# Kernel optimization log

Measured on AMD Instinct MI355X. Metric: run time of the kernel, lower is better.

Reference implementation:

```python
import jax, jax.numpy as jnp
import numpy as np


def setup_inputs() -> dict:
    key = jax.random.key(0)
    k1, k2, k3 = jax.random.split(key, 3)
    B, N, D, S = 256, 200000, 128, 256
    return {
        "query": jax.random.normal(k1, (B, D), dtype=jnp.float32),
        "keys": jax.random.normal(k2, (N, D), dtype=jnp.float32),
        "slots": jax.random.normal(k3, (N, S), dtype=jnp.float32),
        "k": 8,
    }


def reference(query, keys, slots, k):
    # FAISS IndexFlatIP exact search: inner-product scores over all stored keys.
    scores = jnp.einsum("bd,nd->bn", query, keys)          # [B, N]
    top_scores, top_idx = jax.lax.top_k(scores, k)          # [B, k]
    # Fused id->slot gather (replaces per-(query,neighbor) equality scans).
    retrieved_slots = slots[top_idx]                        # [B, k, slot_dim]
    return retrieved_slots, top_scores
```

## Files before the change

### kernel.cpp

```cpp
#include <hip/hip_runtime.h>

#define NQ    256
#define DD    128
#define NK    200000
#define SD    256
#define KTOP  8
#define CAP   1024

#define NCH   500
#define CHK   400
#define KST   80
#define NST   (CHK/KST)
#define KT    (KST/16)
static_assert(NCH * CHK == NK, "chunking must cover keys");

#define WS_A    0
#define WS_TAUF 65536
#define WS_TAU  66560
#define WS_CNT  67584
#define WS_FLAG 68608
#define WS_CAND 69632

#define NEG_INF (-3.402823466e+38f)

typedef __attribute__((ext_vector_type(8))) short short8;
typedef __attribute__((ext_vector_type(4))) float f32x4;

__device__ __forceinline__ unsigned f2bf(float f) {
    unsigned u = __float_as_uint(f);
    u += 0x7fffu + ((u >> 16) & 1u);
    return u >> 16;
}

__device__ __forceinline__ float dot128(const float4* __restrict__ qr,
                                        const float4* __restrict__ kr) {
    float s0 = 0.f, s1 = 0.f;
#pragma unroll
    for (int d = 0; d < 16; ++d) {
        float4 a = qr[d], b = kr[d];
        s0 = fmaf(a.x, b.x, s0); s0 = fmaf(a.y, b.y, s0);
        s0 = fmaf(a.z, b.z, s0); s0 = fmaf(a.w, b.w, s0);
    }
#pragma unroll
    for (int d = 16; d < 32; ++d) {
        float4 a = qr[d], b = kr[d];
        s1 = fmaf(a.x, b.x, s1); s1 = fmaf(a.y, b.y, s1);
        s1 = fmaf(a.z, b.z, s1); s1 = fmaf(a.w, b.w, s1);
    }
    return s0 + s1;
}

template <int T>
__device__ __forceinline__ void topk_insert(float (&vs)[T], int (&vi)[T],
                                            float &vmin, float s, int idx) {
    if (s <= vmin) return;
    bool done = false;
#pragma unroll
    for (int j = 0; j < T; ++j)
        if (!done && vs[j] == vmin) { vs[j] = s; vi[j] = idx; done = true; }
    float m = vs[0];
#pragma unroll
    for (int j = 1; j < T; ++j) m = fminf(m, vs[j]);
    vmin = m;
}

__device__ void finalize_write(int q, int t, float (&vs)[KTOP], int (&vi)[KTOP],
                               float vmin, float* ds, int* di,
                               const float* __restrict__ slots,
                               float* __restrict__ out) {
#pragma unroll
    for (int j = 0; j < KTOP; ++j) { ds[t * KTOP + j] = vs[j]; di[t * KTOP + j] = vi[j]; }
    __syncthreads();
    for (int step = 128; step >= 1; step >>= 1) {
        if (t < step) {
            for (int j = 0; j < KTOP; ++j)
                topk_insert<KTOP>(vs, vi, vmin, ds[(t + step) * KTOP + j],
                                  di[(t + step) * KTOP + j]);
#pragma unroll
            for (int j = 0; j < KTOP; ++j) { ds[t * KTOP + j] = vs[j]; di[t * KTOP + j] = vi[j]; }
        }
        __syncthreads();
    }
    if (t == 0) {
#pragma unroll
        for (int i = 0; i < KTOP; ++i)
#pragma unroll
            for (int j = 0; j < KTOP - 1 - i; ++j) {
                bool swp = (vs[j + 1] > vs[j]) ||
                           (vs[j + 1] == vs[j] && vi[j + 1] < vi[j]);
                if (swp) {
                    float tf = vs[j]; vs[j] = vs[j + 1]; vs[j + 1] = tf;
                    int   ti = vi[j]; vi[j] = vi[j + 1]; vi[j + 1] = ti;
                }
            }
#pragma unroll
        for (int j = 0; j < KTOP; ++j) { ds[j] = vs[j]; di[j] = vi[j]; }
    }
    __syncthreads();
    const float4* slots4 = (const float4*)slots;
    float4* out4 = (float4*)out;
    for (int f = t; f < KTOP * (SD / 4); f += 256) {
        int j = f >> 6, s4 = f & 63;
        out4[(size_t)q * (KTOP * SD / 4) + f] = slots4[(size_t)di[j] * (SD / 4) + s4];
    }
    if (t < KTOP)
        out[(size_t)NQ * KTOP * SD + q * KTOP + t] = ds[t];
}

__global__ __launch_bounds__(256) void prep(const float* __restrict__ query,
                                            char* __restrict__ ws) {
    __shared__ float qs[16 * DD];
    __shared__ float nrm[16][17];
    const int b = blockIdx.x, t = threadIdx.x;

    const float4* src = (const float4*)(query + (size_t)b * 16 * DD);
    float4* dst = (float4*)qs;
    for (int i = t; i < 512; i += 256) dst[i] = src[i];
    __syncthreads();

    {
        int r = t >> 4, p = t & 15;
        float s = 0.f;
#pragma unroll
        for (int j = 0; j < 8; ++j) { float v = qs[r * DD + p * 8 + j]; s = fmaf(v, v, s); }
        nrm[r][p] = s;
    }
    __syncthreads();
    if (t < 16) {
        float s = 0.f;
#pragma unroll
        for (int p = 0; p < 16; ++p) s += nrm[t][p];
        float tau = 3.2f * sqrtf(s);
        ((float*)(ws + WS_TAU))[b * 16 + t]  = tau;
        ((float*)(ws + WS_TAUF))[b * 16 + t] = tau - 1.0f;
    }
    if (b == 0) { ((int*)(ws + WS_CNT))[t] = 0; ((int*)(ws + WS_FLAG))[t] = 0; }

    {
        int c = t >> 6, l = t & 63, col = l & 15, quad = l >> 4;
        const float* row = qs + col * DD + c * 32 + quad * 8;
        int4 pk;
        pk.x = f2bf(row[0]) | (f2bf(row[1]) << 16);
        pk.y = f2bf(row[2]) | (f2bf(row[3]) << 16);
        pk.z = f2bf(row[4]) | (f2bf(row[5]) << 16);
        pk.w = f2bf(row[6]) | (f2bf(row[7]) << 16);
        ((int4*)(ws + WS_A))[(b * 4 + c) * 64 + l] = pk;
    }
}

__global__ __launch_bounds__(256, 2)
void phaseA(const float* __restrict__ keys, char* __restrict__ ws) {
    __shared__ __align__(16) char sm[KST * 256];

    const int tid = threadIdx.x;
    const int w = tid >> 6, lane = tid & 63;
    const int col = lane & 15, quad = lane >> 4;
    const int key0 = blockIdx.x * CHK;

    const short8* wsA = (const short8*)(ws + WS_A);
    short8 A[4][4];
#pragma unroll
    for (int at = 0; at < 4; ++at)
#pragma unroll
        for (int c = 0; c < 4; ++c)
            A[at][c] = wsA[((w * 4 + at) * 4 + c) * 64 + lane];

    const float* tauf = (const float*)(ws + WS_TAUF);
    float tf[4][4];
#pragma unroll
    for (int at = 0; at < 4; ++at)
#pragma unroll
        for (int r = 0; r < 4; ++r)
            tf[at][r] = tauf[w * 64 + at * 16 + quad * 4 + r];

    int* cnt  = (int*)(ws + WS_CNT);
    int* cand = (int*)(ws + WS_CAND);

    float4 rg[5][2];
#pragma unroll
    for (int i = 0; i < 5; ++i) {
        int u = tid + 256 * i, tc = u >> 6, l = u & 63;
        const float* p = keys + (size_t)(key0 + (tc >> 2) * 16 + (l & 15)) * DD
                              + (tc & 3) * 32 + (l >> 4) * 8;
        rg[i][0] = ((const float4*)p)[0];
        rg[i][1] = ((const float4*)p)[1];
    }

    for (int s = 0; s < NST; ++s) {
#pragma unroll
        for (int i = 0; i < 5; ++i) {
            int u = tid + 256 * i;
            int4 pk;
            pk.x = f2bf(rg[i][0].x) | (f2bf(rg[i][0].y) << 16);
            pk.y = f2bf(rg[i][0].z) | (f2bf(rg[i][0].w) << 16);
            pk.z = f2bf(rg[i][1].x) | (f2bf(rg[i][1].y) << 16);
            pk.w = f2bf(rg[i][1].z) | (f2bf(rg[i][1].w) << 16);
            *(int4*)(sm + (size_t)u * 16) = pk;
        }
        __syncthreads();
        if (s + 1 < NST) {
#pragma unroll
            for (int i = 0; i < 5; ++i) {
                int u = tid + 256 * i, tc = u >> 6, l = u & 63;
                const float* p = keys + (size_t)(key0 + (s + 1) * KST + (tc >> 2) * 16 + (l & 15)) * DD
                                      + (tc & 3) * 32 + (l >> 4) * 8;
                rg[i][0] = ((const float4*)p)[0];
                rg[i][1] = ((const float4*)p)[1];
            }
        }
        const short8* B = (const short8*)sm;
#pragma unroll
        for (int kt = 0; kt < KT; ++kt) {
            short8 b0 = B[(kt * 4 + 0) * 64 + lane];
            short8 b1 = B[(kt * 4 + 1) * 64 + lane];
            short8 b2 = B[(kt * 4 + 2) * 64 + lane];
            short8 b3 = B[(kt * 4 + 3) * 64 + lane];
            const int kidx = key0 + s * KST + kt * 16 + col;
#pragma unroll
            for (int at = 0; at < 4; ++at) {
                f32x4 acc = {0.f, 0.f, 0.f, 0.f};
                acc = __builtin_amdgcn_mfma_f32_16x16x32_bf16(A[at][0], b0, acc, 0, 0, 0);
                acc = __builtin_amdgcn_mfma_f32_16x16x32_bf16(A[at][1], b1, acc, 0, 0, 0);
                acc = __builtin_amdgcn_mfma_f32_16x16x32_bf16(A[at][2], b2, acc, 0, 0, 0);
                acc = __builtin_amdgcn_mfma_f32_16x16x32_bf16(A[at][3], b3, acc, 0, 0, 0);
#pragma unroll
                for (int r = 0; r < 4; ++r) {
                    if (acc[r] > tf[at][r]) {
                        int q = w * 64 + at * 16 + quad * 4 + r;
                        int p = atomicAdd(&cnt[q], 1);
                        if (p < CAP) cand[q * CAP + p] = kidx;
                    }
                }
            }
        }
        __syncthreads();
    }
}

__global__ __launch_bounds__(256)
void phaseB(const float* __restrict__ query, const float* __restrict__ keys,
            const float* __restrict__ slots, float* __restrict__ out,
            char* __restrict__ ws) {
    const int q = blockIdx.x, t = threadIdx.x;

    __shared__ float cs[CAP];
    __shared__ int   ci[CAP];
    __shared__ int   nAbove;
    __shared__ float ds[256 * KTOP];
    __shared__ int   di[256 * KTOP];

    if (t == 0) nAbove = 0;
    __syncthreads();

    const int m0 = ((const int*)(ws + WS_CNT))[q];
    const int m  = min(m0, CAP);
    const float tq = ((const float*)(ws + WS_TAU))[q];
    const int* cand = (const int*)(ws + WS_CAND) + (size_t)q * CAP;
    const float4* qr = (const float4*)(query + (size_t)q * DD);

    int myAbove = 0;
    for (int c = t; c < m; c += 256) {
        int id = cand[c];
        float s = dot128(qr, (const float4*)(keys + (size_t)id * DD));
        cs[c] = s; ci[c] = id;
        if (s >= tq) ++myAbove;
    }
    if (myAbove) atomicAdd(&nAbove, myAbove);
    __syncthreads();

    if (m0 > CAP || nAbove < KTOP) {
        if (t == 0) ((int*)(ws + WS_FLAG))[q] = 1;
        return;
    }

    float vs[KTOP]; int vi[KTOP]; float vmin = NEG_INF;
#pragma unroll
    for (int j = 0; j < KTOP; ++j) { vs[j] = NEG_INF; vi[j] = -1; }
    for (int c = t; c < m; c += 256)
        topk_insert<KTOP>(vs, vi, vmin, cs[c], ci[c]);

    finalize_write(q, t, vs, vi, vmin, ds, di, slots, out);
}

__global__ __launch_bounds__(256)
void fallback(const float* __restrict__ query, const float* __restrict__ keys,
              const float* __restrict__ slots, float* __restrict__ out,
              const char* __restrict__ ws) {
    const int q = blockIdx.x;
    if (((const int*)(ws + WS_FLAG))[q] == 0) return;
    const int t = threadIdx.x;

    __shared__ float ds[256 * KTOP];
    __shared__ int   di[256 * KTOP];

    float vs[KTOP]; int vi[KTOP]; float vmin = NEG_INF;
#pragma unroll
    for (int j = 0; j < KTOP; ++j) { vs[j] = NEG_INF; vi[j] = -1; }

    const float4* qr = (const float4*)(query + (size_t)q * DD);
    for (int id = t; id < NK; id += 256) {
        float s = dot128(qr, (const float4*)(keys + (size_t)id * DD));
        topk_insert<KTOP>(vs, vi, vmin, s, id);
    }
    finalize_write(q, t, vs, vi, vmin, ds, di, slots, out);
}

extern "C" void kernel_launch(void* const* d_in, const int* in_sizes, int n_in,
                              void* d_out, int out_size, void* d_ws, size_t ws_size,
                              hipStream_t stream) {
    const float* query = (const float*)d_in[0];
    const float* keys  = (const float*)d_in[1];
    const float* slots = (const float*)d_in[2];
    (void)in_sizes; (void)n_in; (void)out_size; (void)ws_size;
    char* ws = (char*)d_ws;

    hipLaunchKernelGGL(prep,     dim3(16),  dim3(256), 0, stream, query, ws);
    hipLaunchKernelGGL(phaseA,   dim3(NCH), dim3(256), 0, stream, keys, ws);
    hipLaunchKernelGGL(phaseB,   dim3(NQ),  dim3(256), 0, stream, query, keys, slots,
                       (float*)d_out, ws);
    hipLaunchKernelGGL(fallback, dim3(NQ),  dim3(256), 0, stream, query, keys, slots,
                       (float*)d_out, ws);
}
```

Measured before the change: 367.3 us.

## Double-buffer phaseA LDS stages and fold fallback into phaseB

phaseA now keeps two LDS buffers. The next stage is converted and written into the alternate buffer after the MFMA work, so each stage needs one barrier instead of two. The fallback kernel is removed and its brute-force scan is inlined into phaseB, which drops one kernel launch and the flag workspace. The cost is double the LDS per block, which could limit occupancy at 2 blocks per CU, and phaseB may now carry more register pressure.

```diff
diff --git a/kernel.cpp b/kernel.cpp
--- a/kernel.cpp
+++ b/kernel.cpp
@@ -12,13 +12,13 @@
 #define KST   80
 #define NST   (CHK/KST)
 #define KT    (KST/16)
+#define BUFB  (KST*256)
 static_assert(NCH * CHK == NK, "chunking must cover keys");
 
 #define WS_A    0
 #define WS_TAUF 65536
 #define WS_TAU  66560
 #define WS_CNT  67584
-#define WS_FLAG 68608
 #define WS_CAND 69632
 
 #define NEG_INF (-3.402823466e+38f)
@@ -134,7 +134,7 @@
         ((float*)(ws + WS_TAU))[b * 16 + t]  = tau;
         ((float*)(ws + WS_TAUF))[b * 16 + t] = tau - 1.0f;
     }
-    if (b == 0) { ((int*)(ws + WS_CNT))[t] = 0; ((int*)(ws + WS_FLAG))[t] = 0; }
+    if (b == 0) ((int*)(ws + WS_CNT))[t] = 0;
 
     {
         int c = t >> 6, l = t & 63, col = l & 15, quad = l >> 4;
@@ -150,7 +150,7 @@
 
 __global__ __launch_bounds__(256, 2)
 void phaseA(const float* __restrict__ keys, char* __restrict__ ws) {
-    __shared__ __align__(16) char sm[KST * 256];
+    __shared__ __align__(16) char sm[2 * BUFB];
 
     const int tid = threadIdx.x;
     const int w = tid >> 6, lane = tid & 63;
@@ -177,38 +177,40 @@
     int* cand = (int*)(ws + WS_CAND);
 
     float4 rg[5][2];
-#pragma unroll
-    for (int i = 0; i < 5; ++i) {
-        int u = tid + 256 * i, tc = u >> 6, l = u & 63;
-        const float* p = keys + (size_t)(key0 + (tc >> 2) * 16 + (l & 15)) * DD
-                              + (tc & 3) * 32 + (l >> 4) * 8;
-        rg[i][0] = ((const float4*)p)[0];
-        rg[i][1] = ((const float4*)p)[1];
-    }
+
+#define LOAD_STAGE(S)                                                          \
+    {                                                                          \
+        _Pragma("unroll")                                                      \
+        for (int i = 0; i < 5; ++i) {                                          \
+            int u = tid + 256 * i, tc = u >> 6, l = u & 63;                    \
+            const float* p = keys +                                            \
+                (size_t)(key0 + (S) * KST + (tc >> 2) * 16 + (l & 15)) * DD +  \
+                (tc & 3) * 32 + (l >> 4) * 8;                                  \
+            rg[i][0] = ((const float4*)p)[0];                                  \
+            rg[i][1] = ((const float4*)p)[1];                                  \
+        }                                                                      \
+    }
+#define WRITE_STAGE(BUF)                                                       \
+    {                                                                          \
+        _Pragma("unroll")                                                      \
+        for (int i = 0; i < 5; ++i) {                                          \
+            int u = tid + 256 * i;                                             \
+            int4 pk;                                                           \
+            pk.x = f2bf(rg[i][0].x) | (f2bf(rg[i][0].y) << 16);                \
+            pk.y = f2bf(rg[i][0].z) | (f2bf(rg[i][0].w) << 16);                \
+            pk.z = f2bf(rg[i][1].x) | (f2bf(rg[i][1].y) << 16);                \
+            pk.w = f2bf(rg[i][1].z) | (f2bf(rg[i][1].w) << 16);                \
+            *(int4*)(sm + (size_t)(BUF) * BUFB + (size_t)u * 16) = pk;         \
+        }                                                                      \
+    }
+
+    LOAD_STAGE(0);
+    WRITE_STAGE(0);
+    __syncthreads();
 
     for (int s = 0; s < NST; ++s) {
-#pragma unroll
-        for (int i = 0; i < 5; ++i) {
-            int u = tid + 256 * i;
-            int4 pk;
-            pk.x = f2bf(rg[i][0].x) | (f2bf(rg[i][0].y) << 16);
-            pk.y = f2bf(rg[i][0].z) | (f2bf(rg[i][0].w) << 16);
-            pk.z = f2bf(rg[i][1].x) | (f2bf(rg[i][1].y) << 16);
-            pk.w = f2bf(rg[i][1].z) | (f2bf(rg[i][1].w) << 16);
-            *(int4*)(sm + (size_t)u * 16) = pk;
-        }
-        __syncthreads();
-        if (s + 1 < NST) {
-#pragma unroll
-            for (int i = 0; i < 5; ++i) {
-                int u = tid + 256 * i, tc = u >> 6, l = u & 63;
-                const float* p = keys + (size_t)(key0 + (s + 1) * KST + (tc >> 2) * 16 + (l & 15)) * DD
-                                      + (tc & 3) * 32 + (l >> 4) * 8;
-                rg[i][0] = ((const float4*)p)[0];
-                rg[i][1] = ((const float4*)p)[1];
-            }
-        }
-        const short8* B = (const short8*)sm;
+        if (s + 1 < NST) LOAD_STAGE(s + 1);
+        const short8* B = (const short8*)(sm + (s & 1) * BUFB);
 #pragma unroll
         for (int kt = 0; kt < KT; ++kt) {
             short8 b0 = B[(kt * 4 + 0) * 64 + lane];
@@ -233,8 +235,13 @@
                 }
             }
         }
-        __syncthreads();
-    }
+        if (s + 1 < NST) {
+            WRITE_STAGE((s + 1) & 1);
+            __syncthreads();
+        }
+    }
+#undef LOAD_STAGE
+#undef WRITE_STAGE
 }
 
 __global__ __launch_bounds__(256)
@@ -268,40 +275,20 @@
     if (myAbove) atomicAdd(&nAbove, myAbove);
     __syncthreads();
 
+    float vs[KTOP]; int vi[KTOP]; float vmin = NEG_INF;
+#pragma unroll
+    for (int j = 0; j < KTOP; ++j) { vs[j] = NEG_INF; vi[j] = -1; }
+
     if (m0 > CAP || nAbove < KTOP) {
-        if (t == 0) ((int*)(ws + WS_FLAG))[q] = 1;
-        return;
-    }
-
-    float vs[KTOP]; int vi[KTOP]; float vmin = NEG_INF;
-#pragma unroll
-    for (int j = 0; j < KTOP; ++j) { vs[j] = NEG_INF; vi[j] = -1; }
-    for (int c = t; c < m; c += 256)
-        topk_insert<KTOP>(vs, vi, vmin, cs[c], ci[c]);
-
-    finalize_write(q, t, vs, vi, vmin, ds, di, slots, out);
-}
-
-__global__ __launch_bounds__(256)
-void fallback(const float* __restrict__ query, const float* __restrict__ keys,
-              const float* __restrict__ slots, float* __restrict__ out,
-              const char* __restrict__ ws) {
-    const int q = blockIdx.x;
-    if (((const int*)(ws + WS_FLAG))[q] == 0) return;
-    const int t = threadIdx.x;
-
-    __shared__ float ds[256 * KTOP];
-    __shared__ int   di[256 * KTOP];
-
-    float vs[KTOP]; int vi[KTOP]; float vmin = NEG_INF;
-#pragma unroll
-    for (int j = 0; j < KTOP; ++j) { vs[j] = NEG_INF; vi[j] = -1; }
-
-    const float4* qr = (const float4*)(query + (size_t)q * DD);
-    for (int id = t; id < NK; id += 256) {
-        float s = dot128(qr, (const float4*)(keys + (size_t)id * DD));
-        topk_insert<KTOP>(vs, vi, vmin, s, id);
-    }
+        for (int id = t; id < NK; id += 256) {
+            float s = dot128(qr, (const float4*)(keys + (size_t)id * DD));
+            topk_insert<KTOP>(vs, vi, vmin, s, id);
+        }
+    } else {
+        for (int c = t; c < m; c += 256)
+            topk_insert<KTOP>(vs, vi, vmin, cs[c], ci[c]);
+    }
+
     finalize_write(q, t, vs, vi, vmin, ds, di, slots, out);
 }
 
@@ -314,10 +301,8 @@
     (void)in_sizes; (void)n_in; (void)out_size; (void)ws_size;
     char* ws = (char*)d_ws;
 
-    hipLaunchKernelGGL(prep,     dim3(16),  dim3(256), 0, stream, query, ws);
-    hipLaunchKernelGGL(phaseA,   dim3(NCH), dim3(256), 0, stream, keys, ws);
-    hipLaunchKernelGGL(phaseB,   dim3(NQ),  dim3(256), 0, stream, query, keys, slots,
+    hipLaunchKernelGGL(prep,   dim3(16),  dim3(256), 0, stream, query, ws);
+    hipLaunchKernelGGL(phaseA, dim3(NCH), dim3(256), 0, stream, keys, ws);
+    hipLaunchKernelGGL(phaseB, dim3(NQ),  dim3(256), 0, stream, query, keys, slots,
                        (float*)d_out, ws);
-    hipLaunchKernelGGL(fallback, dim3(NQ),  dim3(256), 0, stream, query, keys, slots,
-                       (float*)d_out, ws);
-}
+}
```

Result: no change. 365.2 us (-0.6%).
